# Optimization experiments

Measured on AMD Instinct MI355X. Metric: run time of the kernel, lower is better.

The kernel has to match this reference:

```python
import jax, jax.numpy as jnp
import numpy as np

N_NODES = 50000
N_EDGES = 800000
NUM_GRAPHS = 256
EPS = 1e-5


def _gcn_conv(x, edge_index, W, b):
    # PyG GCNConv: add self-loops, sym-normalize, aggregate, then add bias.
    n = x.shape[0]
    xw = x @ W  # [N, out]
    loops = jnp.arange(n)
    row = jnp.concatenate([edge_index[0], loops])  # source
    col = jnp.concatenate([edge_index[1], loops])  # target
    deg = jax.ops.segment_sum(jnp.ones_like(col, dtype=xw.dtype), col, num_segments=n)
    dinv = jnp.where(deg > 0, jax.lax.rsqrt(deg), 0.0)
    norm = dinv[row] * dinv[col]  # [E+N]
    msg = norm[:, None] * xw[row]  # gather + scale
    out = jax.ops.segment_sum(msg, col, num_segments=n)  # scatter-add
    return out + b


def _bn(x, g, b, m, v):
    # inference-mode batch norm
    return (x - m) * jax.lax.rsqrt(v + EPS) * g + b


def reference(x, edge_index, batch, gcn_W0, gcn_b0, bn_g0, bn_b0, bn_m0, bn_v0,
              gcn_W1, gcn_b1, bn_g1, bn_b1, bn_m1, bn_v1,
              hW1, hb1, hg1, hbb1, hm1, hv1,
              hW2, hb2, hg2, hbb2, hm2, hv2,
              hW3, hb3, hW4, hb4):
    # GCN block 0
    h = _gcn_conv(x, edge_index, gcn_W0, gcn_b0)
    h = jax.nn.relu(_bn(h, bn_g0, bn_b0, bn_m0, bn_v0))  # dropout = identity (eval)
    # GCN block 1
    h = _gcn_conv(h, edge_index, gcn_W1, gcn_b1)
    h = jax.nn.relu(_bn(h, bn_g1, bn_b1, bn_m1, bn_v1))
    # global mean pool over graphs
    sums = jax.ops.segment_sum(h, batch, num_segments=NUM_GRAPHS)
    cnts = jax.ops.segment_sum(jnp.ones_like(batch, dtype=h.dtype), batch, num_segments=NUM_GRAPHS)
    pooled = sums / jnp.maximum(cnts, 1.0)[:, None]  # [G, 64]
    # MLP head (eval: dropout identity)
    z = jax.nn.relu(_bn(pooled @ hW1 + hb1, hg1, hbb1, hm1, hv1))
    z = jax.nn.relu(_bn(z @ hW2 + hb2, hg2, hbb2, hm2, hv2))
    z = jax.nn.relu(z @ hW3 + hb3)
    out = (z @ hW4 + hb4).reshape(-1)  # [G]
    return out


def setup_inputs() -> dict:
    key = jax.random.key(0)
    ks = jax.random.split(key, 12)
    d = 64
    inp = {
        'x': jax.random.normal(ks[0], (N_NODES, d), dtype=jnp.float32),
        'edge_index': jax.random.randint(ks[1], (2, N_EDGES), 0, N_NODES, dtype=jnp.int64),
        'batch': jnp.sort(jax.random.randint(ks[2], (N_NODES,), 0, NUM_GRAPHS, dtype=jnp.int64)),
        'gcn_W0': jax.random.normal(ks[3], (d, d), dtype=jnp.float32) * 0.1,
        'gcn_b0': jnp.zeros((d,), jnp.float32),
        'bn_g0': jnp.ones((d,), jnp.float32), 'bn_b0': jnp.zeros((d,), jnp.float32),
        'bn_m0': jnp.zeros((d,), jnp.float32), 'bn_v0': jnp.ones((d,), jnp.float32),
        'gcn_W1': jax.random.normal(ks[4], (d, d), dtype=jnp.float32) * 0.1,
        'gcn_b1': jnp.zeros((d,), jnp.float32),
        'bn_g1': jnp.ones((d,), jnp.float32), 'bn_b1': jnp.zeros((d,), jnp.float32),
        'bn_m1': jnp.zeros((d,), jnp.float32), 'bn_v1': jnp.ones((d,), jnp.float32),
        'hW1': jax.random.normal(ks[5], (d, 256), dtype=jnp.float32) * 0.1,
        'hb1': jnp.zeros((256,), jnp.float32),
        'hg1': jnp.ones((256,), jnp.float32), 'hbb1': jnp.zeros((256,), jnp.float32),
        'hm1': jnp.zeros((256,), jnp.float32), 'hv1': jnp.ones((256,), jnp.float32),
        'hW2': jax.random.normal(ks[6], (256, 128), dtype=jnp.float32) * 0.1,
        'hb2': jnp.zeros((128,), jnp.float32),
        'hg2': jnp.ones((128,), jnp.float32), 'hbb2': jnp.zeros((128,), jnp.float32),
        'hm2': jnp.zeros((128,), jnp.float32), 'hv2': jnp.ones((128,), jnp.float32),
        'hW3': jax.random.normal(ks[7], (128, 64), dtype=jnp.float32) * 0.1,
        'hb3': jnp.zeros((64,), jnp.float32),
        'hW4': jax.random.normal(ks[8], (64, 1), dtype=jnp.float32) * 0.1,
        'hb4': jnp.zeros((1,), jnp.float32),
    }
    return inp
```

## Files before the change

kernel.cpp:

```cpp
#include <hip/hip_runtime.h>
#include <hip/hip_bf16.h>
#include <hip/hip_fp16.h>

#define N_NODES 50000
#define N_EDGES 800000
#define NUM_GRAPHS 256
#define D 64
#define EPS 1e-5f
#define N_PART 8
#define PART_SIZE (N_NODES / N_PART)
#define SCAT_CHUNKS 512
#define SCAT_GRID (SCAT_CHUNKS * N_PART)
#define GEMM_BLOCKS ((N_NODES + 63) / 64)
#define WP 72

typedef _Float16 half8_t __attribute__((ext_vector_type(8)));
typedef _Float16 half4_t __attribute__((ext_vector_type(4)));
typedef float f32x4 __attribute__((ext_vector_type(4)));

__device__ __forceinline__ void acc16(const uint4& v, float w, float4& A, float4& B) {
    const __half2* hp = (const __half2*)&v;
    float2 q0 = __half22float2(hp[0]), q1 = __half22float2(hp[1]);
    float2 q2 = __half22float2(hp[2]), q3 = __half22float2(hp[3]);
    A.x += w * q0.x; A.y += w * q0.y; A.z += w * q1.x; A.w += w * q1.y;
    B.x += w * q2.x; B.y += w * q2.y; B.z += w * q3.x; B.w += w * q3.y;
}

__global__ __launch_bounds__(256) void build_gemm_kernel(
        const int* __restrict__ ei, int* __restrict__ cnt,
        unsigned short* __restrict__ ssrc, int cap,
        const float* __restrict__ X, const float* __restrict__ W,
        __half* __restrict__ Yh) {
    __shared__ _Float16 Xs[64 * WP];
    __shared__ _Float16 Wt[64 * WP];
    if (blockIdx.x >= GEMM_BLOCKS) {
        int scat  = blockIdx.x - GEMM_BLOCKS;
        int p     = blockIdx.x & (N_PART - 1);
        int chunk = scat >> 3;
        const int per = (((N_EDGES + SCAT_CHUNKS - 1) / SCAT_CHUNKS) + 3) & ~3;
        int lo = chunk * per;
        int hi = lo + per; if (hi > N_EDGES) hi = N_EDGES;
        for (int e4 = lo + (int)threadIdx.x * 4; e4 < hi; e4 += 1024) {
            int4 c4 = *(const int4*)&ei[N_EDGES + e4];
            const int* cc = (const int*)&c4;
#pragma unroll
            for (int k = 0; k < 4; k++) {
                int e = e4 + k;
                if (e < hi) {
                    int c = cc[k];
                    if (c / PART_SIZE == p) {
                        int r = ei[e];
                        int pos = atomicAdd(&cnt[c], 1);
                        if (pos < cap) ssrc[(size_t)c * cap + pos] = (unsigned short)r;
                    }
                }
            }
        }
        return;
    }
    int tid  = threadIdx.x;
    int base = blockIdx.x * 64;
    for (int i = tid; i < 4096; i += 256) {
        int k = i >> 6, n = i & 63;
        Wt[n * WP + k] = (_Float16)W[i];
    }
    for (int i = tid; i < 1024; i += 256) {
        int r = i >> 4, c4 = (i & 15) * 4;
        f32x4 xv;
        if (base + r < N_NODES) {
            xv = __builtin_nontemporal_load(
                     &((const f32x4*)X)[(size_t)(base + r) * 16 + (i & 15)]);
        } else {
            xv = (f32x4){0.f, 0.f, 0.f, 0.f};
        }
        _Float16* dst = &Xs[r * WP + c4];
        dst[0] = (_Float16)xv.x; dst[1] = (_Float16)xv.y;
        dst[2] = (_Float16)xv.z; dst[3] = (_Float16)xv.w;
    }
    __syncthreads();
    int wave  = tid >> 6;
    int lane  = tid & 63;
    int m     = lane & 15;
    int q     = lane >> 4;
    int row16 = wave * 16;
    half8_t a0 = *(const half8_t*)&Xs[(row16 + m) * WP + q * 8];
    half8_t a1 = *(const half8_t*)&Xs[(row16 + m) * WP + 32 + q * 8];
    f32x4 acc[4];
#pragma unroll
    for (int ct = 0; ct < 4; ct++) {
        half8_t b0 = *(const half8_t*)&Wt[(ct * 16 + m) * WP + q * 8];
        half8_t b1 = *(const half8_t*)&Wt[(ct * 16 + m) * WP + 32 + q * 8];
        f32x4 c = {0.f, 0.f, 0.f, 0.f};
        c = __builtin_amdgcn_mfma_f32_16x16x32_f16(a0, b0, c, 0, 0, 0);
        c = __builtin_amdgcn_mfma_f32_16x16x32_f16(a1, b1, c, 0, 0, 0);
        acc[ct] = c;
    }
#pragma unroll
    for (int ct = 0; ct < 4; ct++) {
#pragma unroll
        for (int reg = 0; reg < 4; reg++) {
            int row = base + row16 + q * 4 + reg;
            if (row < N_NODES)
                Yh[(size_t)row * 64 + ct * 16 + m] = (__half)acc[ct][reg];
        }
    }
}

template<bool OUTF16>
__global__ __launch_bounds__(256) void agg_bn_kernel(
        const __half* __restrict__ xwh, const int* __restrict__ cnt,
        const unsigned short* __restrict__ ssrc, int cap,
        const float* __restrict__ b, const float* __restrict__ g,
        const float* __restrict__ bb, const float* __restrict__ m,
        const float* __restrict__ var,
        void* __restrict__ out, int N) {
    int wave = (blockIdx.x * blockDim.x + threadIdx.x) >> 6;
    int lane = threadIdx.x & 63;
    if (wave >= N) return;
    int c   = wave;
    int sub = lane >> 3;
    int f2  = lane & 7;
    const uint4* xw8 = (const uint4*)xwh;
    int n = cnt[c];
    if (n > cap) n = cap;
    float dc = rsqrtf((float)n + 1.0f);
    size_t sbase = (size_t)c * cap;
    int idx = (lane < cap) ? (int)ssrc[sbase + lane] : 0;
    uint4 vself = make_uint4(0u, 0u, 0u, 0u);
    if (sub == 0) vself = xw8[(size_t)c * 8 + f2];
    int t = (n + 7) >> 3;
    float4 accA = make_float4(0.f, 0.f, 0.f, 0.f);
    float4 accB = accA;

    uint4 v0 = make_uint4(0u,0u,0u,0u), v1 = v0;
    int   cv0 = -1, cv1 = -1;
    auto issue = [&](int k, uint4& v, int& cv) {
        int s = k * 8 + sub;
        int sc = (s < n) ? s : 0;
        int r  = __shfl(idx, sc, 64);
        if (s >= n) r = c;
        cv = (s < n) ? cnt[r] : -1;
        v  = xw8[(size_t)r * 8 + f2];
    };
    auto consume = [&](const uint4& v, int cv) {
        if (cv >= 0) acc16(v, rsqrtf((float)cv + 1.0f), accA, accB);
    };
    if (t > 0) issue(0, v0, cv0);
    if (t > 1) issue(1, v1, cv1);
    for (int k = 0; k < t; k++) {
        consume(v0, cv0);
        v0 = v1; cv0 = cv1;
        if (k + 2 < t) issue(k + 2, v1, cv1); else cv1 = -1;
    }
    if (sub == 0) acc16(vself, dc, accA, accB);
#pragma unroll
    for (int off = 8; off < 64; off <<= 1) {
        accA.x += __shfl_xor(accA.x, off, 64); accA.y += __shfl_xor(accA.y, off, 64);
        accA.z += __shfl_xor(accA.z, off, 64); accA.w += __shfl_xor(accA.w, off, 64);
        accB.x += __shfl_xor(accB.x, off, 64); accB.y += __shfl_xor(accB.y, off, 64);
        accB.z += __shfl_xor(accB.z, off, 64); accB.w += __shfl_xor(accB.w, off, 64);
    }
    if (sub < 2) {
        int i4 = 2 * f2 + sub;
        float4 acc = sub ? accB : accA;
        float4 b4  = ((const float4*)b)[i4];
        float4 m4  = ((const float4*)m)[i4];
        float4 v4_ = ((const float4*)var)[i4];
        float4 g4  = ((const float4*)g)[i4];
        float4 bb4 = ((const float4*)bb)[i4];
        float4 h;
        h.x = (acc.x * dc + b4.x - m4.x) * (1.0f / sqrtf(v4_.x + EPS)) * g4.x + bb4.x;
        h.y = (acc.y * dc + b4.y - m4.y) * (1.0f / sqrtf(v4_.y + EPS)) * g4.y + bb4.y;
        h.z = (acc.z * dc + b4.z - m4.z) * (1.0f / sqrtf(v4_.z + EPS)) * g4.z + bb4.z;
        h.w = (acc.w * dc + b4.w - m4.w) * (1.0f / sqrtf(v4_.w + EPS)) * g4.w + bb4.w;
        h.x = h.x > 0.f ? h.x : 0.f;
        h.y = h.y > 0.f ? h.y : 0.f;
        h.z = h.z > 0.f ? h.z : 0.f;
        h.w = h.w > 0.f ? h.w : 0.f;
        if (OUTF16) {
            half4_t hv = {(_Float16)h.x, (_Float16)h.y, (_Float16)h.z, (_Float16)h.w};
            *(half4_t*)((__half*)out + (size_t)c * 64 + i4 * 4) = hv;
        } else {
            ((float4*)out)[(size_t)c * 16 + i4] = h;
        }
    }
}

__global__ __launch_bounds__(256) void gemm64h_kernel(const __half* __restrict__ Xh,
                                                      const float* __restrict__ W,
                                                      __half* __restrict__ Yh, int N) {
    __shared__ _Float16 Xs[64 * WP];
    __shared__ _Float16 Wt[64 * WP];
    int tid  = threadIdx.x;
    int base = blockIdx.x * 64;
    for (int i = tid; i < 4096; i += 256) {
        int k = i >> 6, n = i & 63;
        Wt[n * WP + k] = (_Float16)W[i];
    }
    for (int i = tid; i < 512; i += 256) {
        int r = i >> 3, c8 = (i & 7) * 8;
        uint4 v = (base + r < N)
            ? ((const uint4*)Xh)[(size_t)(base + r) * 8 + (i & 7)]
            : make_uint4(0u, 0u, 0u, 0u);
        *(uint4*)&Xs[r * WP + c8] = v;
    }
    __syncthreads();
    int wave  = tid >> 6;
    int lane  = tid & 63;
    int m     = lane & 15;
    int q     = lane >> 4;
    int row16 = wave * 16;
    half8_t a0 = *(const half8_t*)&Xs[(row16 + m) * WP + q * 8];
    half8_t a1 = *(const half8_t*)&Xs[(row16 + m) * WP + 32 + q * 8];
    f32x4 acc[4];
#pragma unroll
    for (int ct = 0; ct < 4; ct++) {
        half8_t b0 = *(const half8_t*)&Wt[(ct * 16 + m) * WP + q * 8];
        half8_t b1 = *(const half8_t*)&Wt[(ct * 16 + m) * WP + 32 + q * 8];
        f32x4 c = {0.f, 0.f, 0.f, 0.f};
        c = __builtin_amdgcn_mfma_f32_16x16x32_f16(a0, b0, c, 0, 0, 0);
        c = __builtin_amdgcn_mfma_f32_16x16x32_f16(a1, b1, c, 0, 0, 0);
        acc[ct] = c;
    }
#pragma unroll
    for (int ct = 0; ct < 4; ct++) {
#pragma unroll
        for (int reg = 0; reg < 4; reg++) {
            int row = base + row16 + q * 4 + reg;
            if (row < N)
                Yh[(size_t)row * 64 + ct * 16 + m] = (__half)acc[ct][reg];
        }
    }
}

__global__ __launch_bounds__(256) void pool_head_kernel(
        const float* __restrict__ h, const int* __restrict__ batch,
        const float* __restrict__ hW1, const float* __restrict__ hb1,
        const float* __restrict__ hg1, const float* __restrict__ hbb1,
        const float* __restrict__ hm1, const float* __restrict__ hv1,
        const float* __restrict__ hW2, const float* __restrict__ hb2,
        const float* __restrict__ hg2, const float* __restrict__ hbb2,
        const float* __restrict__ hm2, const float* __restrict__ hv2,
        const float* __restrict__ hW3, const float* __restrict__ hb3,
        const float* __restrict__ hW4, const float* __restrict__ hb4,
        float* __restrict__ out) {
    __shared__ int se[2];
    __shared__ float red[256];
    __shared__ float pooled[64];
    __shared__ float z1[256];
    __shared__ float z2[128];
    __shared__ float z3[64];
    int g = blockIdx.x;
    int t = threadIdx.x;
    if (t < 2) {
        int target = g + t;
        int lo = 0, hi = N_NODES;
        while (lo < hi) {
            int mid = (lo + hi) >> 1;
            if (batch[mid] < target) lo = mid + 1; else hi = mid;
        }
        se[t] = lo;
    }
    __syncthreads();
    int start = se[0], end = se[1];
    {
        int f = t & 63, rg = t >> 6;
        float part = 0.0f;
        for (int r = start + rg; r < end; r += 4) part += h[(size_t)r * 64 + f];
        red[t] = part;
        __syncthreads();
        if (t < 64) {
            float s = red[t] + red[t + 64] + red[t + 128] + red[t + 192];
            float cnt = (float)(end - start);
            cnt = cnt > 1.0f ? cnt : 1.0f;
            pooled[t] = s / cnt;
        }
    }
    __syncthreads();
    {
        float acc = hb1[t];
#pragma unroll
        for (int k = 0; k < 64; k++) acc += pooled[k] * hW1[k * 256 + t];
        acc = (acc - hm1[t]) * (1.0f / sqrtf(hv1[t] + EPS)) * hg1[t] + hbb1[t];
        z1[t] = acc > 0.0f ? acc : 0.0f;
    }
    __syncthreads();
    if (t < 128) {
        float acc = hb2[t];
#pragma unroll 8
        for (int k = 0; k < 256; k++) acc += z1[k] * hW2[k * 128 + t];
        acc = (acc - hm2[t]) * (1.0f / sqrtf(hv2[t] + EPS)) * hg2[t] + hbb2[t];
        z2[t] = acc > 0.0f ? acc : 0.0f;
    }
    __syncthreads();
    if (t < 64) {
        float acc = hb3[t];
#pragma unroll 8
        for (int k = 0; k < 128; k++) acc += z2[k] * hW3[k * 64 + t];
        z3[t] = acc > 0.0f ? acc : 0.0f;
    }
    __syncthreads();
    if (t < 64) {
        float v = z3[t] * hW4[t];
        for (int off = 32; off > 0; off >>= 1) v += __shfl_down(v, off, 64);
        if (t == 0) out[g] = v + hb4[0];
    }
}

extern "C" void kernel_launch(void* const* d_in, const int* in_sizes, int n_in,
                              void* d_out, int out_size, void* d_ws, size_t ws_size,
                              hipStream_t stream) {
    const float* x     = (const float*)d_in[0];
    const int*   ei    = (const int*)d_in[1];
    const int*   batch = (const int*)d_in[2];
    const float* W0 = (const float*)d_in[3];
    const float* b0 = (const float*)d_in[4];
    const float* g0 = (const float*)d_in[5];
    const float* bb0 = (const float*)d_in[6];
    const float* m0 = (const float*)d_in[7];
    const float* v0 = (const float*)d_in[8];
    const float* W1 = (const float*)d_in[9];
    const float* b1 = (const float*)d_in[10];
    const float* g1 = (const float*)d_in[11];
    const float* bb1 = (const float*)d_in[12];
    const float* m1 = (const float*)d_in[13];
    const float* v1 = (const float*)d_in[14];
    const float* hW1 = (const float*)d_in[15];
    const float* hb1 = (const float*)d_in[16];
    const float* hg1 = (const float*)d_in[17];
    const float* hbb1 = (const float*)d_in[18];
    const float* hm1 = (const float*)d_in[19];
    const float* hv1 = (const float*)d_in[20];
    const float* hW2 = (const float*)d_in[21];
    const float* hb2 = (const float*)d_in[22];
    const float* hg2 = (const float*)d_in[23];
    const float* hbb2 = (const float*)d_in[24];
    const float* hm2 = (const float*)d_in[25];
    const float* hv2 = (const float*)d_in[26];
    const float* hW3 = (const float*)d_in[27];
    const float* hb3 = (const float*)d_in[28];
    const float* hW4 = (const float*)d_in[29];
    const float* hb4 = (const float*)d_in[30];
    float* out = (float*)d_out;

    __half* xwhA = (__half*)d_ws;
    __half* xwhB = xwhA + (size_t)N_NODES * D;
    float*  bufB = (float*)(xwhB + (size_t)N_NODES * D);
    int*    cnt  = (int*)(bufB + (size_t)N_NODES * D);
    unsigned short* ssrc = (unsigned short*)(cnt + N_NODES);

    size_t used = (size_t)2 * N_NODES * D * 2 + (size_t)N_NODES * D * 4
                + (size_t)N_NODES * 4;
    int cap = 64;
    if (ws_size >= used) {
        size_t avail = (ws_size - used) / ((size_t)N_NODES * 2);
        if (avail < (size_t)cap) cap = (int)avail & ~7;
    } else {
        cap = 0;
    }

    const int NT = 256;
    hipMemsetAsync(cnt, 0, (size_t)N_NODES * 4, stream);

    build_gemm_kernel<<<SCAT_GRID + GEMM_BLOCKS, NT, 0, stream>>>(
        ei, cnt, ssrc, cap, x, W0, xwhA);

    agg_bn_kernel<true><<<(N_NODES * 64) / NT, NT, 0, stream>>>(
        xwhA, cnt, ssrc, cap, b0, g0, bb0, m0, v0, xwhB, N_NODES);

    gemm64h_kernel<<<GEMM_BLOCKS, NT, 0, stream>>>(xwhB, W1, xwhA, N_NODES);

    agg_bn_kernel<false><<<(N_NODES * 64) / NT, NT, 0, stream>>>(
        xwhA, cnt, ssrc, cap, b1, g1, bb1, m1, v1, bufB, N_NODES);

    pool_head_kernel<<<NUM_GRAPHS, NT, 0, stream>>>(bufB, batch,
        hW1, hb1, hg1, hbb1, hm1, hv1,
        hW2, hb2, hg2, hbb2, hm2, hv2,
        hW3, hb3, hW4, hb4, out);
}
```

Baseline: 258.2 us.

## Fuse second aggregation with mean-pool and prescale rows by source degree

The second GEMM now multiplies each output row by its own rsqrt(deg+1), so the layer-1 aggregation no longer needs a per-edge cnt lookup. The second aggregation is also fused with global mean pooling. Each 1024-thread block handles 16 nodes, reduces them into shared-memory per-graph sums with shared atomics, then flushes to global sums with atomics. This removes the fp32 N×64 intermediate write and read and the per-graph serial pooling loop, at the cost of global atomic contention and a different floating-point summation order.

```diff
diff --git a/kernel.cpp b/kernel.cpp
--- a/kernel.cpp
+++ b/kernel.cpp
@@ -13,6 +13,8 @@
 #define SCAT_GRID (SCAT_CHUNKS * N_PART)
 #define GEMM_BLOCKS ((N_NODES + 63) / 64)
 #define WP 72
+#define POOL_NODES 16
+#define POOL_BLOCKS (N_NODES / POOL_NODES)
 
 typedef _Float16 half8_t __attribute__((ext_vector_type(8)));
 typedef _Float16 half4_t __attribute__((ext_vector_type(4)));
@@ -24,6 +26,74 @@
     float2 q2 = __half22float2(hp[2]), q3 = __half22float2(hp[3]);
     A.x += w * q0.x; A.y += w * q0.y; A.z += w * q1.x; A.w += w * q1.y;
     B.x += w * q2.x; B.y += w * q2.y; B.z += w * q3.x; B.w += w * q3.y;
+}
+
+template<bool PRESCALED>
+__device__ __forceinline__ void agg_core(const uint4* __restrict__ xw8,
+        const int* __restrict__ cnt, const unsigned short* __restrict__ ssrc,
+        int cap, int c, int lane, float4& accA, float4& accB, float& dc) {
+    int sub = lane >> 3;
+    int f2  = lane & 7;
+    int n = cnt[c];
+    if (n > cap) n = cap;
+    dc = rsqrtf((float)n + 1.0f);
+    size_t sbase = (size_t)c * cap;
+    int idx = (lane < cap) ? (int)ssrc[sbase + lane] : 0;
+    uint4 vself = make_uint4(0u, 0u, 0u, 0u);
+    if (sub == 0) vself = xw8[(size_t)c * 8 + f2];
+    int t = (n + 7) >> 3;
+    accA = make_float4(0.f, 0.f, 0.f, 0.f);
+    accB = accA;
+    uint4 v0 = make_uint4(0u,0u,0u,0u), v1 = v0;
+    int   cv0 = -1, cv1 = -1;
+    auto issue = [&](int k, uint4& v, int& cv) {
+        int s = k * 8 + sub;
+        int sc = (s < n) ? s : 0;
+        int r  = __shfl(idx, sc, 64);
+        if (s >= n) r = c;
+        if (PRESCALED) cv = (s < n) ? 0 : -1;
+        else           cv = (s < n) ? cnt[r] : -1;
+        v = xw8[(size_t)r * 8 + f2];
+    };
+    auto consume = [&](const uint4& v, int cv) {
+        if (cv >= 0) acc16(v, PRESCALED ? 1.0f : rsqrtf((float)cv + 1.0f), accA, accB);
+    };
+    if (t > 0) issue(0, v0, cv0);
+    if (t > 1) issue(1, v1, cv1);
+    for (int k = 0; k < t; k++) {
+        consume(v0, cv0);
+        v0 = v1; cv0 = cv1;
+        if (k + 2 < t) issue(k + 2, v1, cv1); else cv1 = -1;
+    }
+    if (sub == 0) acc16(vself, PRESCALED ? 1.0f : dc, accA, accB);
+#pragma unroll
+    for (int off = 8; off < 64; off <<= 1) {
+        accA.x += __shfl_xor(accA.x, off, 64); accA.y += __shfl_xor(accA.y, off, 64);
+        accA.z += __shfl_xor(accA.z, off, 64); accA.w += __shfl_xor(accA.w, off, 64);
+        accB.x += __shfl_xor(accB.x, off, 64); accB.y += __shfl_xor(accB.y, off, 64);
+        accB.z += __shfl_xor(accB.z, off, 64); accB.w += __shfl_xor(accB.w, off, 64);
+    }
+}
+
+__device__ __forceinline__ float4 bn_relu4(float4 acc, float dc, int i4,
+        const float* __restrict__ b, const float* __restrict__ g,
+        const float* __restrict__ bb, const float* __restrict__ m,
+        const float* __restrict__ var) {
+    float4 b4  = ((const float4*)b)[i4];
+    float4 m4  = ((const float4*)m)[i4];
+    float4 v4_ = ((const float4*)var)[i4];
+    float4 g4  = ((const float4*)g)[i4];
+    float4 bb4 = ((const float4*)bb)[i4];
+    float4 h;
+    h.x = (acc.x * dc + b4.x - m4.x) * (1.0f / sqrtf(v4_.x + EPS)) * g4.x + bb4.x;
+    h.y = (acc.y * dc + b4.y - m4.y) * (1.0f / sqrtf(v4_.y + EPS)) * g4.y + bb4.y;
+    h.z = (acc.z * dc + b4.z - m4.z) * (1.0f / sqrtf(v4_.z + EPS)) * g4.z + bb4.z;
+    h.w = (acc.w * dc + b4.w - m4.w) * (1.0f / sqrtf(v4_.w + EPS)) * g4.w + bb4.w;
+    h.x = h.x > 0.f ? h.x : 0.f;
+    h.y = h.y > 0.f ? h.y : 0.f;
+    h.z = h.z > 0.f ? h.z : 0.f;
+    h.w = h.w > 0.f ? h.w : 0.f;
+    return h;
 }
 
 __global__ __launch_bounds__(256) void build_gemm_kernel(
@@ -106,88 +176,31 @@
     }
 }
 
-template<bool OUTF16>
 __global__ __launch_bounds__(256) void agg_bn_kernel(
         const __half* __restrict__ xwh, const int* __restrict__ cnt,
         const unsigned short* __restrict__ ssrc, int cap,
         const float* __restrict__ b, const float* __restrict__ g,
         const float* __restrict__ bb, const float* __restrict__ m,
         const float* __restrict__ var,
-        void* __restrict__ out, int N) {
+        __half* __restrict__ out, int N) {
     int wave = (blockIdx.x * blockDim.x + threadIdx.x) >> 6;
     int lane = threadIdx.x & 63;
     if (wave >= N) return;
-    int c   = wave;
-    int sub = lane >> 3;
-    int f2  = lane & 7;
-    const uint4* xw8 = (const uint4*)xwh;
-    int n = cnt[c];
-    if (n > cap) n = cap;
-    float dc = rsqrtf((float)n + 1.0f);
-    size_t sbase = (size_t)c * cap;
-    int idx = (lane < cap) ? (int)ssrc[sbase + lane] : 0;
-    uint4 vself = make_uint4(0u, 0u, 0u, 0u);
-    if (sub == 0) vself = xw8[(size_t)c * 8 + f2];
-    int t = (n + 7) >> 3;
-    float4 accA = make_float4(0.f, 0.f, 0.f, 0.f);
-    float4 accB = accA;
-
-    uint4 v0 = make_uint4(0u,0u,0u,0u), v1 = v0;
-    int   cv0 = -1, cv1 = -1;
-    auto issue = [&](int k, uint4& v, int& cv) {
-        int s = k * 8 + sub;
-        int sc = (s < n) ? s : 0;
-        int r  = __shfl(idx, sc, 64);
-        if (s >= n) r = c;
-        cv = (s < n) ? cnt[r] : -1;
-        v  = xw8[(size_t)r * 8 + f2];
-    };
-    auto consume = [&](const uint4& v, int cv) {
-        if (cv >= 0) acc16(v, rsqrtf((float)cv + 1.0f), accA, accB);
-    };
-    if (t > 0) issue(0, v0, cv0);
-    if (t > 1) issue(1, v1, cv1);
-    for (int k = 0; k < t; k++) {
-        consume(v0, cv0);
-        v0 = v1; cv0 = cv1;
-        if (k + 2 < t) issue(k + 2, v1, cv1); else cv1 = -1;
-    }
-    if (sub == 0) acc16(vself, dc, accA, accB);
-#pragma unroll
-    for (int off = 8; off < 64; off <<= 1) {
-        accA.x += __shfl_xor(accA.x, off, 64); accA.y += __shfl_xor(accA.y, off, 64);
-        accA.z += __shfl_xor(accA.z, off, 64); accA.w += __shfl_xor(accA.w, off, 64);
-        accB.x += __shfl_xor(accB.x, off, 64); accB.y += __shfl_xor(accB.y, off, 64);
-        accB.z += __shfl_xor(accB.z, off, 64); accB.w += __shfl_xor(accB.w, off, 64);
-    }
+    int c = wave;
+    float4 accA, accB; float dc;
+    agg_core<false>((const uint4*)xwh, cnt, ssrc, cap, c, lane, accA, accB, dc);
+    int sub = lane >> 3, f2 = lane & 7;
     if (sub < 2) {
         int i4 = 2 * f2 + sub;
-        float4 acc = sub ? accB : accA;
-        float4 b4  = ((const float4*)b)[i4];
-        float4 m4  = ((const float4*)m)[i4];
-        float4 v4_ = ((const float4*)var)[i4];
-        float4 g4  = ((const float4*)g)[i4];
-        float4 bb4 = ((const float4*)bb)[i4];
-        float4 h;
-        h.x = (acc.x * dc + b4.x - m4.x) * (1.0f / sqrtf(v4_.x + EPS)) * g4.x + bb4.x;
-        h.y = (acc.y * dc + b4.y - m4.y) * (1.0f / sqrtf(v4_.y + EPS)) * g4.y + bb4.y;
-        h.z = (acc.z * dc + b4.z - m4.z) * (1.0f / sqrtf(v4_.z + EPS)) * g4.z + bb4.z;
-        h.w = (acc.w * dc + b4.w - m4.w) * (1.0f / sqrtf(v4_.w + EPS)) * g4.w + bb4.w;
-        h.x = h.x > 0.f ? h.x : 0.f;
-        h.y = h.y > 0.f ? h.y : 0.f;
-        h.z = h.z > 0.f ? h.z : 0.f;
-        h.w = h.w > 0.f ? h.w : 0.f;
-        if (OUTF16) {
-            half4_t hv = {(_Float16)h.x, (_Float16)h.y, (_Float16)h.z, (_Float16)h.w};
-            *(half4_t*)((__half*)out + (size_t)c * 64 + i4 * 4) = hv;
-        } else {
-            ((float4*)out)[(size_t)c * 16 + i4] = h;
-        }
+        float4 h = bn_relu4(sub ? accB : accA, dc, i4, b, g, bb, m, var);
+        half4_t hv = {(_Float16)h.x, (_Float16)h.y, (_Float16)h.z, (_Float16)h.w};
+        *(half4_t*)(out + (size_t)c * 64 + i4 * 4) = hv;
     }
 }
 
 __global__ __launch_bounds__(256) void gemm64h_kernel(const __half* __restrict__ Xh,
                                                       const float* __restrict__ W,
+                                                      const int* __restrict__ cnt,
                                                       __half* __restrict__ Yh, int N) {
     __shared__ _Float16 Xs[64 * WP];
     __shared__ _Float16 Wt[64 * WP];
@@ -222,19 +235,68 @@
         c = __builtin_amdgcn_mfma_f32_16x16x32_f16(a1, b1, c, 0, 0, 0);
         acc[ct] = c;
     }
+    int   rows[4];
+    float ws[4];
+#pragma unroll
+    for (int reg = 0; reg < 4; reg++) {
+        rows[reg] = base + row16 + q * 4 + reg;
+        ws[reg] = (rows[reg] < N) ? rsqrtf((float)cnt[rows[reg]] + 1.0f) : 0.0f;
+    }
 #pragma unroll
     for (int ct = 0; ct < 4; ct++) {
 #pragma unroll
         for (int reg = 0; reg < 4; reg++) {
-            int row = base + row16 + q * 4 + reg;
-            if (row < N)
-                Yh[(size_t)row * 64 + ct * 16 + m] = (__half)acc[ct][reg];
-        }
-    }
-}
-
-__global__ __launch_bounds__(256) void pool_head_kernel(
-        const float* __restrict__ h, const int* __restrict__ batch,
+            if (rows[reg] < N)
+                Yh[(size_t)rows[reg] * 64 + ct * 16 + m] =
+                    (__half)(ws[reg] * acc[ct][reg]);
+        }
+    }
+}
+
+__global__ __launch_bounds__(1024) void agg_pool_kernel(
+        const __half* __restrict__ xwh, const int* __restrict__ cnt,
+        const unsigned short* __restrict__ ssrc, int cap,
+        const float* __restrict__ b, const float* __restrict__ g,
+        const float* __restrict__ bb, const float* __restrict__ m,
+        const float* __restrict__ var,
+        const int* __restrict__ batch, float* __restrict__ sums, int N) {
+    __shared__ float gsum[POOL_NODES][64];
+    __shared__ int ginfo[2];
+    int tid  = threadIdx.x;
+    int base = blockIdx.x * POOL_NODES;
+    gsum[tid >> 6][tid & 63] = 0.0f;
+    if (tid == 0) {
+        int last = base + POOL_NODES - 1; if (last >= N) last = N - 1;
+        ginfo[0] = batch[base];
+        ginfo[1] = batch[last] - batch[base] + 1;
+    }
+    __syncthreads();
+    int glo = ginfo[0], span = ginfo[1];
+    int wave = tid >> 6, lane = tid & 63;
+    int c = base + wave;
+    if (c < N) {
+        float4 accA, accB; float dc;
+        agg_core<true>((const uint4*)xwh, cnt, ssrc, cap, c, lane, accA, accB, dc);
+        int sub = lane >> 3, f2 = lane & 7;
+        if (sub < 2) {
+            int i4 = 2 * f2 + sub;
+            float4 h = bn_relu4(sub ? accB : accA, dc, i4, b, g, bb, m, var);
+            int sp = batch[c] - glo;
+            float* gp = &gsum[sp][i4 * 4];
+            atomicAdd(&gp[0], h.x); atomicAdd(&gp[1], h.y);
+            atomicAdd(&gp[2], h.z); atomicAdd(&gp[3], h.w);
+        }
+    }
+    __syncthreads();
+    for (int i = tid; i < span * 64; i += 1024) {
+        float v = gsum[i >> 6][i & 63];
+        if (v != 0.0f || true)
+            atomicAdd(&sums[(size_t)(glo + (i >> 6)) * 64 + (i & 63)], v);
+    }
+}
+
+__global__ __launch_bounds__(256) void head_kernel(
+        const float* __restrict__ sums, const int* __restrict__ batch,
         const float* __restrict__ hW1, const float* __restrict__ hb1,
         const float* __restrict__ hg1, const float* __restrict__ hbb1,
         const float* __restrict__ hm1, const float* __restrict__ hv1,
@@ -245,7 +307,6 @@
         const float* __restrict__ hW4, const float* __restrict__ hb4,
         float* __restrict__ out) {
     __shared__ int se[2];
-    __shared__ float red[256];
     __shared__ float pooled[64];
     __shared__ float z1[256];
     __shared__ float z2[128];
@@ -262,19 +323,10 @@
         se[t] = lo;
     }
     __syncthreads();
-    int start = se[0], end = se[1];
-    {
-        int f = t & 63, rg = t >> 6;
-        float part = 0.0f;
-        for (int r = start + rg; r < end; r += 4) part += h[(size_t)r * 64 + f];
-        red[t] = part;
-        __syncthreads();
-        if (t < 64) {
-            float s = red[t] + red[t + 64] + red[t + 128] + red[t + 192];
-            float cnt = (float)(end - start);
-            cnt = cnt > 1.0f ? cnt : 1.0f;
-            pooled[t] = s / cnt;
-        }
+    if (t < 64) {
+        float cntf = (float)(se[1] - se[0]);
+        cntf = cntf > 1.0f ? cntf : 1.0f;
+        pooled[t] = sums[(size_t)g * 64 + t] / cntf;
     }
     __syncthreads();
     {
@@ -345,12 +397,12 @@
 
     __half* xwhA = (__half*)d_ws;
     __half* xwhB = xwhA + (size_t)N_NODES * D;
-    float*  bufB = (float*)(xwhB + (size_t)N_NODES * D);
-    int*    cnt  = (int*)(bufB + (size_t)N_NODES * D);
-    unsigned short* ssrc = (unsigned short*)(cnt + N_NODES);
-
-    size_t used = (size_t)2 * N_NODES * D * 2 + (size_t)N_NODES * D * 4
-                + (size_t)N_NODES * 4;
+    int*    cnt  = (int*)(xwhB + (size_t)N_NODES * D);
+    float*  sums = (float*)(cnt + N_NODES);
+    unsigned short* ssrc = (unsigned short*)(sums + NUM_GRAPHS * D);
+
+    size_t used = (size_t)2 * N_NODES * D * 2 + (size_t)N_NODES * 4
+                + (size_t)NUM_GRAPHS * D * 4;
     int cap = 64;
     if (ws_size >= used) {
         size_t avail = (ws_size - used) / ((size_t)N_NODES * 2);
@@ -360,20 +412,21 @@
     }
 
     const int NT = 256;
-    hipMemsetAsync(cnt, 0, (size_t)N_NODES * 4, stream);
+    (void)hipMemsetAsync(cnt, 0, (size_t)N_NODES * 4 + (size_t)NUM_GRAPHS * D * 4,
+                         stream);
 
     build_gemm_kernel<<<SCAT_GRID + GEMM_BLOCKS, NT, 0, stream>>>(
         ei, cnt, ssrc, cap, x, W0, xwhA);
 
-    agg_bn_kernel<true><<<(N_NODES * 64) / NT, NT, 0, stream>>>(
+    agg_bn_kernel<<<(N_NODES * 64) / NT, NT, 0, stream>>>(
         xwhA, cnt, ssrc, cap, b0, g0, bb0, m0, v0, xwhB, N_NODES);
 
-    gemm64h_kernel<<<GEMM_BLOCKS, NT, 0, stream>>>(xwhB, W1, xwhA, N_NODES);
-
-    agg_bn_kernel<false><<<(N_NODES * 64) / NT, NT, 0, stream>>>(
-        xwhA, cnt, ssrc, cap, b1, g1, bb1, m1, v1, bufB, N_NODES);
-
-    pool_head_kernel<<<NUM_GRAPHS, NT, 0, stream>>>(bufB, batch,
+    gemm64h_kernel<<<GEMM_BLOCKS, NT, 0, stream>>>(xwhB, W1, cnt, xwhA, N_NODES);
+
+    agg_pool_kernel<<<POOL_BLOCKS, 1024, 0, stream>>>(
+        xwhA, cnt, ssrc, cap, b1, g1, bb1, m1, v1, batch, sums, N_NODES);
+
+    head_kernel<<<NUM_GRAPHS, NT, 0, stream>>>(sums, batch,
         hW1, hb1, hg1, hbb1, hm1, hv1,
         hW2, hb2, hg2, hbb2, hm2, hv2,
         hW3, hb3, hW4, hb4, out);
```

Measured after the change: 266.8 us. +3.3%, slower.

## Pre-scale rows by source degree norm and simplify edge scatter

Applied to the files above, without the earlier changes.

Folds the source-side normalization dinv[row] into the features ahead of aggregation. A new scale kernel handles layer 0, and the second GEMM's epilogue handles layer 1. The aggregation loop then no longer gathers cnt[r] or computes an rsqrt per neighbor. The edge scatter also drops the 8-way partitioned pass over all edges in favour of one pass, where each thread handles four edges with vector loads for both row and col. The cost is an extra launch and a read/write of the layer-0 features, plus more atomic contention and less locality in the scatter.

```diff
diff --git a/kernel.cpp b/kernel.cpp
--- a/kernel.cpp
+++ b/kernel.cpp
@@ -7,23 +7,83 @@
 #define NUM_GRAPHS 256
 #define D 64
 #define EPS 1e-5f
-#define N_PART 8
-#define PART_SIZE (N_NODES / N_PART)
-#define SCAT_CHUNKS 512
-#define SCAT_GRID (SCAT_CHUNKS * N_PART)
 #define GEMM_BLOCKS ((N_NODES + 63) / 64)
+#define SCAT_BLOCKS ((N_EDGES + 1023) / 1024)
 #define WP 72
 
 typedef _Float16 half8_t __attribute__((ext_vector_type(8)));
 typedef _Float16 half4_t __attribute__((ext_vector_type(4)));
 typedef float f32x4 __attribute__((ext_vector_type(4)));
 
-__device__ __forceinline__ void acc16(const uint4& v, float w, float4& A, float4& B) {
+__device__ __forceinline__ void acc16(const uint4& v, float4& A, float4& B) {
     const __half2* hp = (const __half2*)&v;
     float2 q0 = __half22float2(hp[0]), q1 = __half22float2(hp[1]);
     float2 q2 = __half22float2(hp[2]), q3 = __half22float2(hp[3]);
-    A.x += w * q0.x; A.y += w * q0.y; A.z += w * q1.x; A.w += w * q1.y;
-    B.x += w * q2.x; B.y += w * q2.y; B.z += w * q3.x; B.w += w * q3.y;
+    A.x += q0.x; A.y += q0.y; A.z += q1.x; A.w += q1.y;
+    B.x += q2.x; B.y += q2.y; B.z += q3.x; B.w += q3.y;
+}
+
+__device__ __forceinline__ void agg_core(const uint4* __restrict__ xw8,
+        const int* __restrict__ cnt, const unsigned short* __restrict__ ssrc,
+        int cap, int c, int lane, float4& accA, float4& accB, float& dc) {
+    int sub = lane >> 3;
+    int f2  = lane & 7;
+    int n = cnt[c];
+    if (n > cap) n = cap;
+    dc = rsqrtf((float)n + 1.0f);
+    size_t sbase = (size_t)c * cap;
+    int idx = (lane < cap) ? (int)ssrc[sbase + lane] : 0;
+    uint4 vself = make_uint4(0u, 0u, 0u, 0u);
+    if (sub == 0) vself = xw8[(size_t)c * 8 + f2];
+    int t = (n + 7) >> 3;
+    accA = make_float4(0.f, 0.f, 0.f, 0.f);
+    accB = accA;
+    uint4 v0 = make_uint4(0u,0u,0u,0u), v1 = v0;
+    bool  ok0 = false, ok1 = false;
+    auto issue = [&](int k, uint4& v, bool& ok) {
+        int s = k * 8 + sub;
+        int sc = (s < n) ? s : 0;
+        int r  = __shfl(idx, sc, 64);
+        if (s >= n) r = c;
+        ok = (s < n);
+        v = xw8[(size_t)r * 8 + f2];
+    };
+    if (t > 0) issue(0, v0, ok0);
+    if (t > 1) issue(1, v1, ok1);
+    for (int k = 0; k < t; k++) {
+        if (ok0) acc16(v0, accA, accB);
+        v0 = v1; ok0 = ok1;
+        if (k + 2 < t) issue(k + 2, v1, ok1); else ok1 = false;
+    }
+    if (sub == 0) acc16(vself, accA, accB);
+#pragma unroll
+    for (int off = 8; off < 64; off <<= 1) {
+        accA.x += __shfl_xor(accA.x, off, 64); accA.y += __shfl_xor(accA.y, off, 64);
+        accA.z += __shfl_xor(accA.z, off, 64); accA.w += __shfl_xor(accA.w, off, 64);
+        accB.x += __shfl_xor(accB.x, off, 64); accB.y += __shfl_xor(accB.y, off, 64);
+        accB.z += __shfl_xor(accB.z, off, 64); accB.w += __shfl_xor(accB.w, off, 64);
+    }
+}
+
+__device__ __forceinline__ float4 bn_relu4(float4 acc, float dc, int i4,
+        const float* __restrict__ b, const float* __restrict__ g,
+        const float* __restrict__ bb, const float* __restrict__ m,
+        const float* __restrict__ var) {
+    float4 b4  = ((const float4*)b)[i4];
+    float4 m4  = ((const float4*)m)[i4];
+    float4 v4_ = ((const float4*)var)[i4];
+    float4 g4  = ((const float4*)g)[i4];
+    float4 bb4 = ((const float4*)bb)[i4];
+    float4 h;
+    h.x = (acc.x * dc + b4.x - m4.x) * (1.0f / sqrtf(v4_.x + EPS)) * g4.x + bb4.x;
+    h.y = (acc.y * dc + b4.y - m4.y) * (1.0f / sqrtf(v4_.y + EPS)) * g4.y + bb4.y;
+    h.z = (acc.z * dc + b4.z - m4.z) * (1.0f / sqrtf(v4_.z + EPS)) * g4.z + bb4.z;
+    h.w = (acc.w * dc + b4.w - m4.w) * (1.0f / sqrtf(v4_.w + EPS)) * g4.w + bb4.w;
+    h.x = h.x > 0.f ? h.x : 0.f;
+    h.y = h.y > 0.f ? h.y : 0.f;
+    h.z = h.z > 0.f ? h.z : 0.f;
+    h.w = h.w > 0.f ? h.w : 0.f;
+    return h;
 }
 
 __global__ __launch_bounds__(256) void build_gemm_kernel(
@@ -34,25 +94,20 @@
     __shared__ _Float16 Xs[64 * WP];
     __shared__ _Float16 Wt[64 * WP];
     if (blockIdx.x >= GEMM_BLOCKS) {
-        int scat  = blockIdx.x - GEMM_BLOCKS;
-        int p     = blockIdx.x & (N_PART - 1);
-        int chunk = scat >> 3;
-        const int per = (((N_EDGES + SCAT_CHUNKS - 1) / SCAT_CHUNKS) + 3) & ~3;
-        int lo = chunk * per;
-        int hi = lo + per; if (hi > N_EDGES) hi = N_EDGES;
-        for (int e4 = lo + (int)threadIdx.x * 4; e4 < hi; e4 += 1024) {
+        int sb = blockIdx.x - GEMM_BLOCKS;
+        int e4 = (sb * 256 + (int)threadIdx.x) * 4;
+        if (e4 < N_EDGES) {
+            int4 r4 = *(const int4*)&ei[e4];
             int4 c4 = *(const int4*)&ei[N_EDGES + e4];
+            const int* rr = (const int*)&r4;
             const int* cc = (const int*)&c4;
 #pragma unroll
             for (int k = 0; k < 4; k++) {
                 int e = e4 + k;
-                if (e < hi) {
+                if (e < N_EDGES) {
                     int c = cc[k];
-                    if (c / PART_SIZE == p) {
-                        int r = ei[e];
-                        int pos = atomicAdd(&cnt[c], 1);
-                        if (pos < cap) ssrc[(size_t)c * cap + pos] = (unsigned short)r;
-                    }
+                    int pos = atomicAdd(&cnt[c], 1);
+                    if (pos < cap) ssrc[(size_t)c * cap + pos] = (unsigned short)rr[k];
                 }
             }
         }
@@ -104,6 +159,23 @@
                 Yh[(size_t)row * 64 + ct * 16 + m] = (__half)acc[ct][reg];
         }
     }
+}
+
+__global__ __launch_bounds__(256) void scale_kernel(__half* __restrict__ xwh,
+                                                    const int* __restrict__ cnt,
+                                                    int N) {
+    int i = blockIdx.x * 256 + threadIdx.x;
+    if (i >= N * 8) return;
+    int row = i >> 3;
+    float w = rsqrtf((float)cnt[row] + 1.0f);
+    uint4 v = ((const uint4*)xwh)[i];
+    __half2* hp = (__half2*)&v;
+#pragma unroll
+    for (int j = 0; j < 4; j++) {
+        float2 q = __half22float2(hp[j]);
+        hp[j] = __floats2half2_rn(q.x * w, q.y * w);
+    }
+    ((uint4*)xwh)[i] = v;
 }
 
 template<bool OUTF16>
@@ -117,66 +189,13 @@
     int wave = (blockIdx.x * blockDim.x + threadIdx.x) >> 6;
     int lane = threadIdx.x & 63;
     if (wave >= N) return;
-    int c   = wave;
-    int sub = lane >> 3;
-    int f2  = lane & 7;
-    const uint4* xw8 = (const uint4*)xwh;
-    int n = cnt[c];
-    if (n > cap) n = cap;
-    float dc = rsqrtf((float)n + 1.0f);
-    size_t sbase = (size_t)c * cap;
-    int idx = (lane < cap) ? (int)ssrc[sbase + lane] : 0;
-    uint4 vself = make_uint4(0u, 0u, 0u, 0u);
-    if (sub == 0) vself = xw8[(size_t)c * 8 + f2];
-    int t = (n + 7) >> 3;
-    float4 accA = make_float4(0.f, 0.f, 0.f, 0.f);
-    float4 accB = accA;
-
-    uint4 v0 = make_uint4(0u,0u,0u,0u), v1 = v0;
-    int   cv0 = -1, cv1 = -1;
-    auto issue = [&](int k, uint4& v, int& cv) {
-        int s = k * 8 + sub;
-        int sc = (s < n) ? s : 0;
-        int r  = __shfl(idx, sc, 64);
-        if (s >= n) r = c;
-        cv = (s < n) ? cnt[r] : -1;
-        v  = xw8[(size_t)r * 8 + f2];
-    };
-    auto consume = [&](const uint4& v, int cv) {
-        if (cv >= 0) acc16(v, rsqrtf((float)cv + 1.0f), accA, accB);
-    };
-    if (t > 0) issue(0, v0, cv0);
-    if (t > 1) issue(1, v1, cv1);
-    for (int k = 0; k < t; k++) {
-        consume(v0, cv0);
-        v0 = v1; cv0 = cv1;
-        if (k + 2 < t) issue(k + 2, v1, cv1); else cv1 = -1;
-    }
-    if (sub == 0) acc16(vself, dc, accA, accB);
-#pragma unroll
-    for (int off = 8; off < 64; off <<= 1) {
-        accA.x += __shfl_xor(accA.x, off, 64); accA.y += __shfl_xor(accA.y, off, 64);
-        accA.z += __shfl_xor(accA.z, off, 64); accA.w += __shfl_xor(accA.w, off, 64);
-        accB.x += __shfl_xor(accB.x, off, 64); accB.y += __shfl_xor(accB.y, off, 64);
-        accB.z += __shfl_xor(accB.z, off, 64); accB.w += __shfl_xor(accB.w, off, 64);
-    }
+    int c = wave;
+    float4 accA, accB; float dc;
+    agg_core((const uint4*)xwh, cnt, ssrc, cap, c, lane, accA, accB, dc);
+    int sub = lane >> 3, f2 = lane & 7;
     if (sub < 2) {
         int i4 = 2 * f2 + sub;
-        float4 acc = sub ? accB : accA;
-        float4 b4  = ((const float4*)b)[i4];
-        float4 m4  = ((const float4*)m)[i4];
-        float4 v4_ = ((const float4*)var)[i4];
-        float4 g4  = ((const float4*)g)[i4];
-        float4 bb4 = ((const float4*)bb)[i4];
-        float4 h;
-        h.x = (acc.x * dc + b4.x - m4.x) * (1.0f / sqrtf(v4_.x + EPS)) * g4.x + bb4.x;
-        h.y = (acc.y * dc + b4.y - m4.y) * (1.0f / sqrtf(v4_.y + EPS)) * g4.y + bb4.y;
-        h.z = (acc.z * dc + b4.z - m4.z) * (1.0f / sqrtf(v4_.z + EPS)) * g4.z + bb4.z;
-        h.w = (acc.w * dc + b4.w - m4.w) * (1.0f / sqrtf(v4_.w + EPS)) * g4.w + bb4.w;
-        h.x = h.x > 0.f ? h.x : 0.f;
-        h.y = h.y > 0.f ? h.y : 0.f;
-        h.z = h.z > 0.f ? h.z : 0.f;
-        h.w = h.w > 0.f ? h.w : 0.f;
+        float4 h = bn_relu4(sub ? accB : accA, dc, i4, b, g, bb, m, var);
         if (OUTF16) {
             half4_t hv = {(_Float16)h.x, (_Float16)h.y, (_Float16)h.z, (_Float16)h.w};
             *(half4_t*)((__half*)out + (size_t)c * 64 + i4 * 4) = hv;
@@ -188,6 +207,7 @@
 
 __global__ __launch_bounds__(256) void gemm64h_kernel(const __half* __restrict__ Xh,
                                                       const float* __restrict__ W,
+                                                      const int* __restrict__ cnt,
                                                       __half* __restrict__ Yh, int N) {
     __shared__ _Float16 Xs[64 * WP];
     __shared__ _Float16 Wt[64 * WP];
@@ -222,13 +242,20 @@
         c = __builtin_amdgcn_mfma_f32_16x16x32_f16(a1, b1, c, 0, 0, 0);
         acc[ct] = c;
     }
+    int   rows[4];
+    float ws[4];
+#pragma unroll
+    for (int reg = 0; reg < 4; reg++) {
+        rows[reg] = base + row16 + q * 4 + reg;
+        ws[reg] = (rows[reg] < N) ? rsqrtf((float)cnt[rows[reg]] + 1.0f) : 0.0f;
+    }
 #pragma unroll
     for (int ct = 0; ct < 4; ct++) {
 #pragma unroll
         for (int reg = 0; reg < 4; reg++) {
-            int row = base + row16 + q * 4 + reg;
-            if (row < N)
-                Yh[(size_t)row * 64 + ct * 16 + m] = (__half)acc[ct][reg];
+            if (rows[reg] < N)
+                Yh[(size_t)rows[reg] * 64 + ct * 16 + m] =
+                    (__half)(ws[reg] * acc[ct][reg]);
         }
     }
 }
@@ -360,15 +387,17 @@
     }
 
     const int NT = 256;
-    hipMemsetAsync(cnt, 0, (size_t)N_NODES * 4, stream);
-
-    build_gemm_kernel<<<SCAT_GRID + GEMM_BLOCKS, NT, 0, stream>>>(
+    (void)hipMemsetAsync(cnt, 0, (size_t)N_NODES * 4, stream);
+
+    build_gemm_kernel<<<GEMM_BLOCKS + SCAT_BLOCKS, NT, 0, stream>>>(
         ei, cnt, ssrc, cap, x, W0, xwhA);
+
+    scale_kernel<<<(N_NODES * 8 + NT - 1) / NT, NT, 0, stream>>>(xwhA, cnt, N_NODES);
 
     agg_bn_kernel<true><<<(N_NODES * 64) / NT, NT, 0, stream>>>(
         xwhA, cnt, ssrc, cap, b0, g0, bb0, m0, v0, xwhB, N_NODES);
 
-    gemm64h_kernel<<<GEMM_BLOCKS, NT, 0, stream>>>(xwhB, W1, xwhA, N_NODES);
+    gemm64h_kernel<<<GEMM_BLOCKS, NT, 0, stream>>>(xwhB, W1, cnt, xwhA, N_NODES);
 
     agg_bn_kernel<false><<<(N_NODES * 64) / NT, NT, 0, stream>>>(
         xwhA, cnt, ssrc, cap, b1, g1, bb1, m1, v1, bufB, N_NODES);
```

After: 267.4 us. 1.04x slower.

## Fuse mean-pool into second aggregation via atomics and use nontemporal GEMM stores

Applied to the files above, without the earlier changes.

The second aggregation kernel no longer writes the full fp32 node feature matrix. It atomically adds each node's features into per-graph sums, and the head kernel just divides those sums by the node counts. This removes a 12.8MB write and re-read plus the serial pooling loop, at the cost of 3.2M float atomics contending on 256×64 addresses, with non-deterministic summation order. The GEMM output stores are also switched to nontemporal stores.

```diff
diff --git a/kernel.cpp b/kernel.cpp
--- a/kernel.cpp
+++ b/kernel.cpp
@@ -101,19 +101,21 @@
         for (int reg = 0; reg < 4; reg++) {
             int row = base + row16 + q * 4 + reg;
             if (row < N_NODES)
-                Yh[(size_t)row * 64 + ct * 16 + m] = (__half)acc[ct][reg];
-        }
-    }
-}
-
-template<bool OUTF16>
+                __builtin_nontemporal_store((_Float16)acc[ct][reg],
+                    (_Float16*)&Yh[(size_t)row * 64 + ct * 16 + m]);
+        }
+    }
+}
+
+template<int MODE>
 __global__ __launch_bounds__(256) void agg_bn_kernel(
         const __half* __restrict__ xwh, const int* __restrict__ cnt,
         const unsigned short* __restrict__ ssrc, int cap,
         const float* __restrict__ b, const float* __restrict__ g,
         const float* __restrict__ bb, const float* __restrict__ m,
         const float* __restrict__ var,
-        void* __restrict__ out, int N) {
+        __half* __restrict__ outh, const int* __restrict__ batch,
+        float* __restrict__ sums, int N) {
     int wave = (blockIdx.x * blockDim.x + threadIdx.x) >> 6;
     int lane = threadIdx.x & 63;
     if (wave >= N) return;
@@ -177,11 +179,14 @@
         h.y = h.y > 0.f ? h.y : 0.f;
         h.z = h.z > 0.f ? h.z : 0.f;
         h.w = h.w > 0.f ? h.w : 0.f;
-        if (OUTF16) {
+        if (MODE == 0) {
             half4_t hv = {(_Float16)h.x, (_Float16)h.y, (_Float16)h.z, (_Float16)h.w};
-            *(half4_t*)((__half*)out + (size_t)c * 64 + i4 * 4) = hv;
+            *(half4_t*)(outh + (size_t)c * 64 + i4 * 4) = hv;
         } else {
-            ((float4*)out)[(size_t)c * 16 + i4] = h;
+            int gid = batch[c];
+            float* sp = &sums[(size_t)gid * 64 + i4 * 4];
+            atomicAdd(&sp[0], h.x); atomicAdd(&sp[1], h.y);
+            atomicAdd(&sp[2], h.z); atomicAdd(&sp[3], h.w);
         }
     }
 }
@@ -228,13 +233,14 @@
         for (int reg = 0; reg < 4; reg++) {
             int row = base + row16 + q * 4 + reg;
             if (row < N)
-                Yh[(size_t)row * 64 + ct * 16 + m] = (__half)acc[ct][reg];
-        }
-    }
-}
-
-__global__ __launch_bounds__(256) void pool_head_kernel(
-        const float* __restrict__ h, const int* __restrict__ batch,
+                __builtin_nontemporal_store((_Float16)acc[ct][reg],
+                    (_Float16*)&Yh[(size_t)row * 64 + ct * 16 + m]);
+        }
+    }
+}
+
+__global__ __launch_bounds__(256) void head_kernel(
+        const float* __restrict__ sums, const int* __restrict__ batch,
         const float* __restrict__ hW1, const float* __restrict__ hb1,
         const float* __restrict__ hg1, const float* __restrict__ hbb1,
         const float* __restrict__ hm1, const float* __restrict__ hv1,
@@ -245,7 +251,6 @@
         const float* __restrict__ hW4, const float* __restrict__ hb4,
         float* __restrict__ out) {
     __shared__ int se[2];
-    __shared__ float red[256];
     __shared__ float pooled[64];
     __shared__ float z1[256];
     __shared__ float z2[128];
@@ -262,19 +267,10 @@
         se[t] = lo;
     }
     __syncthreads();
-    int start = se[0], end = se[1];
-    {
-        int f = t & 63, rg = t >> 6;
-        float part = 0.0f;
-        for (int r = start + rg; r < end; r += 4) part += h[(size_t)r * 64 + f];
-        red[t] = part;
-        __syncthreads();
-        if (t < 64) {
-            float s = red[t] + red[t + 64] + red[t + 128] + red[t + 192];
-            float cnt = (float)(end - start);
-            cnt = cnt > 1.0f ? cnt : 1.0f;
-            pooled[t] = s / cnt;
-        }
+    if (t < 64) {
+        float cntf = (float)(se[1] - se[0]);
+        cntf = cntf > 1.0f ? cntf : 1.0f;
+        pooled[t] = sums[(size_t)g * 64 + t] / cntf;
     }
     __syncthreads();
     {
@@ -345,12 +341,12 @@
 
     __half* xwhA = (__half*)d_ws;
     __half* xwhB = xwhA + (size_t)N_NODES * D;
-    float*  bufB = (float*)(xwhB + (size_t)N_NODES * D);
-    int*    cnt  = (int*)(bufB + (size_t)N_NODES * D);
-    unsigned short* ssrc = (unsigned short*)(cnt + N_NODES);
-
-    size_t used = (size_t)2 * N_NODES * D * 2 + (size_t)N_NODES * D * 4
-                + (size_t)N_NODES * 4;
+    int*    cnt  = (int*)(xwhB + (size_t)N_NODES * D);
+    float*  sums = (float*)(cnt + N_NODES);
+    unsigned short* ssrc = (unsigned short*)(sums + NUM_GRAPHS * D);
+
+    size_t used = (size_t)2 * N_NODES * D * 2 + (size_t)N_NODES * 4
+                + (size_t)NUM_GRAPHS * D * 4;
     int cap = 64;
     if (ws_size >= used) {
         size_t avail = (ws_size - used) / ((size_t)N_NODES * 2);
@@ -360,20 +356,21 @@
     }
 
     const int NT = 256;
-    hipMemsetAsync(cnt, 0, (size_t)N_NODES * 4, stream);
+    (void)hipMemsetAsync(cnt, 0, (size_t)N_NODES * 4 + (size_t)NUM_GRAPHS * D * 4,
+                         stream);
 
     build_gemm_kernel<<<SCAT_GRID + GEMM_BLOCKS, NT, 0, stream>>>(
         ei, cnt, ssrc, cap, x, W0, xwhA);
 
-    agg_bn_kernel<true><<<(N_NODES * 64) / NT, NT, 0, stream>>>(
-        xwhA, cnt, ssrc, cap, b0, g0, bb0, m0, v0, xwhB, N_NODES);
+    agg_bn_kernel<0><<<(N_NODES * 64) / NT, NT, 0, stream>>>(
+        xwhA, cnt, ssrc, cap, b0, g0, bb0, m0, v0, xwhB, nullptr, nullptr, N_NODES);
 
     gemm64h_kernel<<<GEMM_BLOCKS, NT, 0, stream>>>(xwhB, W1, xwhA, N_NODES);
 
-    agg_bn_kernel<false><<<(N_NODES * 64) / NT, NT, 0, stream>>>(
-        xwhA, cnt, ssrc, cap, b1, g1, bb1, m1, v1, bufB, N_NODES);
-
-    pool_head_kernel<<<NUM_GRAPHS, NT, 0, stream>>>(bufB, batch,
+    agg_bn_kernel<1><<<(N_NODES * 64) / NT, NT, 0, stream>>>(
+        xwhA, cnt, ssrc, cap, b1, g1, bb1, m1, v1, nullptr, batch, sums, N_NODES);
+
+    head_kernel<<<NUM_GRAPHS, NT, 0, stream>>>(sums, batch,
         hW1, hb1, hg1, hbb1, hm1, hv1,
         hW2, hb2, hg2, hbb2, hm2, hv2,
         hW3, hb3, hW4, hb4, out);
```

Result: slower. 326.1 us (+26.3%).
